# Kernel tuning notes

Measured on AMD Instinct MI355X. Metric: run time of the kernel, lower is better.

Reference implementation:

```python
import jax, jax.numpy as jnp
import numpy as np

# init kwargs baked as constants: crop_height -> depth dim, crop_length -> H, crop_width -> W
CROP_D, CROP_H, CROP_W = 16, 16, 16
EXTRAP = 0.0


def setup_inputs() -> dict:
    key = jax.random.key(0)
    k1, k2, k3 = jax.random.split(key, 3)
    N, C, D, H, W = 8, 32, 64, 64, 64
    NB = 256
    image = jax.random.normal(k1, (N, C, D, H, W), dtype=jnp.float32)
    # boxes: normalized (x1, y1, z1, x2, y2, z2) with lo <= hi per axis
    raw = jax.random.uniform(k2, (NB, 3, 2), dtype=jnp.float32)
    lo = jnp.min(raw, axis=2)
    hi = jnp.max(raw, axis=2)
    boxes = jnp.concatenate([lo, hi], axis=1)  # [NB, 6]
    box_ind = jax.random.randint(k3, (NB,), 0, N, dtype=jnp.int32)
    return {"image": image, "boxes": boxes, "box_ind": box_ind}


def _coords(lo, hi, L, c):
    # lo, hi: [nb] normalized box edges; returns [nb, c] continuous source coords
    if c > 1:
        i = jnp.arange(c, dtype=lo.dtype)
        step = (hi - lo) * (L - 1) / (c - 1)          # [nb]
        return lo[:, None] * (L - 1) + i[None, :] * step[:, None]
    return (0.5 * (lo + hi) * (L - 1))[:, None]


def _lerp_idx(coord, L):
    valid = (coord >= 0) & (coord <= L - 1)
    c = jnp.clip(coord, 0, L - 1)
    i0 = jnp.floor(c).astype(jnp.int32)
    i1 = jnp.minimum(i0 + 1, L - 1)
    frac = c - i0.astype(coord.dtype)
    return i0, i1, frac, valid


def reference(image, boxes, box_ind):
    N, C, D, H, W = image.shape
    x1, y1, z1, x2, y2, z2 = [boxes[:, k] for k in range(6)]
    zc = _coords(z1, z2, D, CROP_D)  # [nb, cd]
    yc = _coords(y1, y2, H, CROP_H)  # [nb, ch]
    xc = _coords(x1, x2, W, CROP_W)  # [nb, cw]
    z0, z1i, fz, vz = _lerp_idx(zc, D)
    y0, y1i, fy, vy = _lerp_idx(yc, H)
    x0, x1i, fx, vx = _lerp_idx(xc, W)

    img = jnp.moveaxis(image, 1, -1)  # [N, D, H, W, C] -> channels-last gather
    b = box_ind[:, None, None, None]

    def g(zi, yi, xi):
        # [nb, cd, ch, cw, C]
        return img[b, zi[:, :, None, None], yi[:, None, :, None], xi[:, None, None, :], :]

    fz_ = fz[:, :, None, None, None]
    fy_ = fy[:, None, :, None, None]
    fx_ = fx[:, None, None, :, None]

    c00 = g(z0, y0, x0) * (1 - fx_) + g(z0, y0, x1i) * fx_
    c01 = g(z0, y1i, x0) * (1 - fx_) + g(z0, y1i, x1i) * fx_
    c10 = g(z1i, y0, x0) * (1 - fx_) + g(z1i, y0, x1i) * fx_
    c11 = g(z1i, y1i, x0) * (1 - fx_) + g(z1i, y1i, x1i) * fx_
    c0 = c00 * (1 - fy_) + c01 * fy_
    c1 = c10 * (1 - fy_) + c11 * fy_
    out = c0 * (1 - fz_) + c1 * fz_  # [nb, cd, ch, cw, C]

    valid = (vz[:, :, None, None] & vy[:, None, :, None] & vx[:, None, None, :])[..., None]
    out = jnp.where(valid, out, jnp.asarray(EXTRAP, out.dtype))
    return jnp.moveaxis(out, -1, 1)  # [nb, C, cd, ch, cw]
```

## Files before the change

kernel.cpp:

```cpp
#include <hip/hip_runtime.h>

#define NBOX 256
#define NC   32
#define ND   64
#define NH   64
#define NW   64
#define CD   16
#define CH   16
#define CW   16
#define NXCD 8
#define HW_  (NH * NW)
#define DHW  (ND * NH * NW)
#define P    68

__global__ __launch_bounds__(256) void CropAndResize3D_89481348645400_kernel(
    const float* __restrict__ image,
    const float* __restrict__ boxes,
    const int*   __restrict__ box_ind,
    float*       __restrict__ out)
{
    __shared__ float sh[2][64 * P];

    const int nwg_per_xcd = (NBOX * CD) / NXCD;
    const int hw  = blockIdx.x;
    const int blk = (hw & (NXCD - 1)) * nwg_per_xcd + (hw >> 3);

    const int b = blk >> 4;
    const int z = blk & 15;
    const int t  = threadIdx.x;
    const int ty = t >> 4;
    const int tx = t & 15;

    const float bx1 = boxes[b*6+0], by1 = boxes[b*6+1], bz1 = boxes[b*6+2];
    const float bx2 = boxes[b*6+3], by2 = boxes[b*6+4], bz2 = boxes[b*6+5];
    const int   n   = box_ind[b];

    const float zstep = (bz2 - bz1) * 63.0f / 15.0f;
    const float ystep = (by2 - by1) * 63.0f / 15.0f;
    const float xstep = (bx2 - bx1) * 63.0f / 15.0f;

    const float zc = bz1 * 63.0f + (float)z * zstep;
    const bool  vz = (zc >= 0.0f) && (zc <= 63.0f);
    const float zq = fminf(fmaxf(zc, 0.0f), 63.0f);
    const int   z0 = (int)floorf(zq);
    const int   z1 = min(z0 + 1, ND - 1);
    const float fz = zq - (float)z0;

    const float yc = by1 * 63.0f + (float)ty * ystep;
    const bool  vy = (yc >= 0.0f) && (yc <= 63.0f);
    const float yq = fminf(fmaxf(yc, 0.0f), 63.0f);
    const float fy = yq - floorf(yq);

    const float xcf = bx1 * 63.0f + (float)tx * xstep;
    const bool  vx  = (xcf >= 0.0f) && (xcf <= 63.0f);
    const float xq  = fminf(fmaxf(xcf, 0.0f), 63.0f);
    const int   x0  = (int)floorf(xq);
    const int   x1  = min(x0 + 1, NW - 1);
    const float fx  = xq - (float)x0;

    const bool valid = vz && vy && vx;
    const float gz = 1.0f - fz, gy = 1.0f - fy, gx = 1.0f - fx;

    const float xcl = bx1 * 63.0f;
    const float xch = bx1 * 63.0f + 15.0f * xstep;
    const int x0min = (int)floorf(fminf(fmaxf(xcl, 0.0f), 63.0f));
    const int x1max = min((int)floorf(fminf(fmaxf(xch, 0.0f), 63.0f)) + 1, NW - 1);
    const int xlo4  = x0min & ~3;
    const int G     = ((x1max - xlo4) >> 2) + 1;
    const bool ld   = (tx < G);

    int soff[4], dst[4];
    #pragma unroll
    for (int k = 0; k < 4; ++k) {
        const int r   = k * 16 + ty;
        const int yo  = (r >> 1) & 15;
        const int yc_ = r & 1;
        const int zs  = (r >> 5) ? z1 : z0;
        const float yco = by1 * 63.0f + (float)yo * ystep;
        const float yqs = fminf(fmaxf(yco, 0.0f), 63.0f);
        const int   ys0 = (int)floorf(yqs);
        const int   ysel = yc_ ? min(ys0 + 1, NH - 1) : ys0;
        soff[k] = (zs * NH + ysel) * NW + xlo4 + tx * 4;
        dst[k]  = r * P + tx * 4;
    }

    const int dx0 = x0 - xlo4;
    const int dx1 = x1 - xlo4;
    const int a00 = (ty * 2 + 0) * P;
    const int a01 = (ty * 2 + 1) * P;
    const int a10 = (32 + ty * 2 + 0) * P;
    const int a11 = (32 + ty * 2 + 1) * P;

    const float* imgb = image + (size_t)n * (NC * DHW);
    float* op = out + (size_t)b * (NC * CD * CH * CW) + (z * CH + ty) * CW + tx;

    float4 A0, A1, A2, A3, B0, B1, B2, B3;

    #define ISSUE(Ra, Rb, Rc, Rd, c)  do { if (ld) {                         \
        const float* p_ = imgb + (size_t)(c) * DHW;                          \
        Ra = *(const float4*)(p_ + soff[0]);                                 \
        Rb = *(const float4*)(p_ + soff[1]);                                 \
        Rc = *(const float4*)(p_ + soff[2]);                                 \
        Rd = *(const float4*)(p_ + soff[3]); } } while (0)

    #define WRITE(Ra, Rb, Rc, Rd, buf)  do { if (ld) {                       \
        *(float4*)(sh[buf] + dst[0]) = Ra;                                   \
        *(float4*)(sh[buf] + dst[1]) = Rb;                                   \
        *(float4*)(sh[buf] + dst[2]) = Rc;                                   \
        *(float4*)(sh[buf] + dst[3]) = Rd; } } while (0)

    #define COMPUTE(buf, c)  do {                                            \
        const float* S_ = sh[buf];                                           \
        const float s000 = S_[a00 + dx0], s001 = S_[a00 + dx1];              \
        const float s010 = S_[a01 + dx0], s011 = S_[a01 + dx1];              \
        const float s100 = S_[a10 + dx0], s101 = S_[a10 + dx1];              \
        const float s110 = S_[a11 + dx0], s111 = S_[a11 + dx1];              \
        const float c00 = s000 * gx + s001 * fx;                             \
        const float c01 = s010 * gx + s011 * fx;                             \
        const float c10 = s100 * gx + s101 * fx;                             \
        const float c11 = s110 * gx + s111 * fx;                             \
        const float c0  = c00 * gy + c01 * fy;                               \
        const float c1  = c10 * gy + c11 * fy;                               \
        float v = c0 * gz + c1 * fz;                                         \
        v = valid ? v : 0.0f;                                                \
        __builtin_nontemporal_store(v, op + (c) * (CD * CH * CW));           \
    } while (0)

    ISSUE(A0, A1, A2, A3, 0);
    WRITE(A0, A1, A2, A3, 0);
    ISSUE(B0, B1, B2, B3, 1);
    __syncthreads();

    for (int c = 0; c < NC; c += 2) {
        if (c + 1 < NC) WRITE(B0, B1, B2, B3, 1);
        if (c + 2 < NC) ISSUE(A0, A1, A2, A3, c + 2);
        COMPUTE(0, c);
        __syncthreads();
        if (c + 1 < NC) {
            if (c + 2 < NC) WRITE(A0, A1, A2, A3, 0);
            if (c + 3 < NC) ISSUE(B0, B1, B2, B3, c + 3);
            COMPUTE(1, c + 1);
            __syncthreads();
        }
    }

    #undef ISSUE
    #undef WRITE
    #undef COMPUTE
}

extern "C" void kernel_launch(void* const* d_in, const int* in_sizes, int n_in,
                              void* d_out, int out_size, void* d_ws, size_t ws_size,
                              hipStream_t stream) {
    const float* image   = (const float*)d_in[0];
    const float* boxes   = (const float*)d_in[1];
    const int*   box_ind = (const int*)d_in[2];
    float*       out     = (float*)d_out;

    const int blocks = NBOX * CD;
    CropAndResize3D_89481348645400_kernel<<<blocks, 256, 0, stream>>>(
        image, boxes, box_ind, out);
}
```

Measured before the change: 124.4 us.

## Load image tiles directly into LDS with global_load_lds and XOR swizzle

Replaces the register-staged global-to-shared copy with direct global-to-LDS loads (global_load_lds, 16 bytes per lane). The padded LDS layout becomes an unpadded 64-wide layout with an XOR swizzle on the 4-float chunk index to avoid bank conflicts. Synchronisation is rewritten to use explicit vmcnt waits and two s_barriers per channel. The aim is to drop the VGPR round trip and the ds_write instructions. The cost is more barriers per iteration, and correctness depends on the wave-uniform LDS base matching the per-lane swizzle arithmetic.

```diff
diff --git a/kernel.cpp b/kernel.cpp
--- a/kernel.cpp
+++ b/kernel.cpp
@@ -1,4 +1,5 @@
 #include <hip/hip_runtime.h>
+#include <stdint.h>
 
 #define NBOX 256
 #define NC   32
@@ -9,9 +10,7 @@
 #define CH   16
 #define CW   16
 #define NXCD 8
-#define HW_  (NH * NW)
 #define DHW  (ND * NH * NW)
-#define P    68
 
 __global__ __launch_bounds__(256) void CropAndResize3D_89481348645400_kernel(
     const float* __restrict__ image,
@@ -19,7 +18,7 @@
     const int*   __restrict__ box_ind,
     float*       __restrict__ out)
 {
-    __shared__ float sh[2][64 * P];
+    __shared__ float sh[2 * 64 * 64];
 
     const int nwg_per_xcd = (NBOX * CD) / NXCD;
     const int hw  = blockIdx.x;
@@ -67,85 +66,106 @@
     const int x1max = min((int)floorf(fminf(fmaxf(xch, 0.0f), 63.0f)) + 1, NW - 1);
     const int xlo4  = x0min & ~3;
     const int G     = ((x1max - xlo4) >> 2) + 1;
-    const bool ld   = (tx < G);
 
-    int soff[4], dst[4];
-    #pragma unroll
-    for (int k = 0; k < 4; ++k) {
-        const int r   = k * 16 + ty;
-        const int yo  = (r >> 1) & 15;
-        const int yc_ = r & 1;
-        const int zs  = (r >> 5) ? z1 : z0;
-        const float yco = by1 * 63.0f + (float)yo * ystep;
-        const float yqs = fminf(fmaxf(yco, 0.0f), 63.0f);
-        const int   ys0 = (int)floorf(yqs);
-        const int   ysel = yc_ ? min(ys0 + 1, NH - 1) : ys0;
-        soff[k] = (zs * NH + ysel) * NW + xlo4 + tx * 4;
-        dst[k]  = r * P + tx * 4;
+    const int key = ty & 7;
+    const bool act = ((tx ^ key) < G);
+    const int sx  = xlo4 + ((tx ^ key) << 2);
+
+    int soff0, soff1, soff2, soff3;
+    {
+        int tmp[4];
+        #pragma unroll
+        for (int k = 0; k < 4; ++k) {
+            const int r   = k * 16 + ty;
+            const int yo  = (r >> 1) & 15;
+            const int yc_ = r & 1;
+            const int zs  = (r >> 5) ? z1 : z0;
+            const float yco = by1 * 63.0f + (float)yo * ystep;
+            const float yqs = fminf(fmaxf(yco, 0.0f), 63.0f);
+            const int   ys0 = (int)floorf(yqs);
+            const int   ysel = yc_ ? min(ys0 + 1, NH - 1) : ys0;
+            tmp[k] = (zs * NH + ysel) * NW + sx;
+        }
+        soff0 = tmp[0]; soff1 = tmp[1]; soff2 = tmp[2]; soff3 = tmp[3];
     }
+    const int wb    = (ty & ~3) * 64;
+    const int ldsb0 = wb;
+    const int ldsb1 = wb + 16 * 64;
+    const int ldsb2 = wb + 32 * 64;
+    const int ldsb3 = wb + 48 * 64;
 
     const int dx0 = x0 - xlo4;
     const int dx1 = x1 - xlo4;
-    const int a00 = (ty * 2 + 0) * P;
-    const int a01 = (ty * 2 + 1) * P;
-    const int a10 = (32 + ty * 2 + 0) * P;
-    const int a11 = (32 + ty * 2 + 1) * P;
+    #define IDX(r, dx) ((r) * 64 + (((((dx) >> 2) ^ ((r) & 7))) << 2) + ((dx) & 3))
+    const int a000 = IDX(2*ty    , dx0), a001 = IDX(2*ty    , dx1);
+    const int a010 = IDX(2*ty + 1, dx0), a011 = IDX(2*ty + 1, dx1);
+    const int a100 = IDX(32+2*ty , dx0), a101 = IDX(32+2*ty , dx1);
+    const int a110 = IDX(33+2*ty , dx0), a111 = IDX(33+2*ty , dx1);
+    #undef IDX
 
     const float* imgb = image + (size_t)n * (NC * DHW);
     float* op = out + (size_t)b * (NC * CD * CH * CW) + (z * CH + ty) * CW + tx;
 
-    float4 A0, A1, A2, A3, B0, B1, B2, B3;
+    #define ISSUE(c)  do { if (act) {                                          \
+        const float* p_ = imgb + (size_t)(c) * DHW;                            \
+        float* l_ = sh + (((c) & 1) << 12);                                    \
+        __builtin_amdgcn_global_load_lds(                                      \
+            (const __attribute__((address_space(1))) uint32_t*)(p_ + soff0),   \
+            (__attribute__((address_space(3))) uint32_t*)(l_ + ldsb0), 16, 0, 0); \
+        __builtin_amdgcn_global_load_lds(                                      \
+            (const __attribute__((address_space(1))) uint32_t*)(p_ + soff1),   \
+            (__attribute__((address_space(3))) uint32_t*)(l_ + ldsb1), 16, 0, 0); \
+        __builtin_amdgcn_global_load_lds(                                      \
+            (const __attribute__((address_space(1))) uint32_t*)(p_ + soff2),   \
+            (__attribute__((address_space(3))) uint32_t*)(l_ + ldsb2), 16, 0, 0); \
+        __builtin_amdgcn_global_load_lds(                                      \
+            (const __attribute__((address_space(1))) uint32_t*)(p_ + soff3),   \
+            (__attribute__((address_space(3))) uint32_t*)(l_ + ldsb3), 16, 0, 0); \
+    } } while (0)
 
-    #define ISSUE(Ra, Rb, Rc, Rd, c)  do { if (ld) {                         \
-        const float* p_ = imgb + (size_t)(c) * DHW;                          \
-        Ra = *(const float4*)(p_ + soff[0]);                                 \
-        Rb = *(const float4*)(p_ + soff[1]);                                 \
-        Rc = *(const float4*)(p_ + soff[2]);                                 \
-        Rd = *(const float4*)(p_ + soff[3]); } } while (0)
-
-    #define WRITE(Ra, Rb, Rc, Rd, buf)  do { if (ld) {                       \
-        *(float4*)(sh[buf] + dst[0]) = Ra;                                   \
-        *(float4*)(sh[buf] + dst[1]) = Rb;                                   \
-        *(float4*)(sh[buf] + dst[2]) = Rc;                                   \
-        *(float4*)(sh[buf] + dst[3]) = Rd; } } while (0)
-
-    #define COMPUTE(buf, c)  do {                                            \
-        const float* S_ = sh[buf];                                           \
-        const float s000 = S_[a00 + dx0], s001 = S_[a00 + dx1];              \
-        const float s010 = S_[a01 + dx0], s011 = S_[a01 + dx1];              \
-        const float s100 = S_[a10 + dx0], s101 = S_[a10 + dx1];              \
-        const float s110 = S_[a11 + dx0], s111 = S_[a11 + dx1];              \
-        const float c00 = s000 * gx + s001 * fx;                             \
-        const float c01 = s010 * gx + s011 * fx;                             \
-        const float c10 = s100 * gx + s101 * fx;                             \
-        const float c11 = s110 * gx + s111 * fx;                             \
-        const float c0  = c00 * gy + c01 * fy;                               \
-        const float c1  = c10 * gy + c11 * fy;                               \
-        float v = c0 * gz + c1 * fz;                                         \
-        v = valid ? v : 0.0f;                                                \
-        __builtin_nontemporal_store(v, op + (c) * (CD * CH * CW));           \
+    #define COMPUTE(c)  do {                                                   \
+        const float* S_ = sh + (((c) & 1) << 12);                              \
+        const float s000 = S_[a000], s001 = S_[a001];                          \
+        const float s010 = S_[a010], s011 = S_[a011];                          \
+        const float s100 = S_[a100], s101 = S_[a101];                          \
+        const float s110 = S_[a110], s111 = S_[a111];                          \
+        const float c00 = s000 * gx + s001 * fx;                               \
+        const float c01 = s010 * gx + s011 * fx;                               \
+        const float c10 = s100 * gx + s101 * fx;                               \
+        const float c11 = s110 * gx + s111 * fx;                               \
+        const float c0  = c00 * gy + c01 * fy;                                 \
+        const float c1  = c10 * gy + c11 * fy;                                 \
+        float v = c0 * gz + c1 * fz;                                           \
+        v = valid ? v : 0.0f;                                                  \
+        __builtin_nontemporal_store(v, op + (c) * (CD * CH * CW));             \
     } while (0)
 
-    ISSUE(A0, A1, A2, A3, 0);
-    WRITE(A0, A1, A2, A3, 0);
-    ISSUE(B0, B1, B2, B3, 1);
-    __syncthreads();
+    ISSUE(0);
+    ISSUE(1);
+    asm volatile("s_waitcnt vmcnt(4)" ::: "memory");
+    __builtin_amdgcn_s_barrier();
+    __builtin_amdgcn_sched_barrier(0);
 
-    for (int c = 0; c < NC; c += 2) {
-        if (c + 1 < NC) WRITE(B0, B1, B2, B3, 1);
-        if (c + 2 < NC) ISSUE(A0, A1, A2, A3, c + 2);
-        COMPUTE(0, c);
-        __syncthreads();
+    #pragma unroll 2
+    for (int c = 0; c < NC; ++c) {
+        COMPUTE(c);
         if (c + 1 < NC) {
-            if (c + 2 < NC) WRITE(A0, A1, A2, A3, 0);
-            if (c + 3 < NC) ISSUE(B0, B1, B2, B3, c + 3);
-            COMPUTE(1, c + 1);
-            __syncthreads();
+            __builtin_amdgcn_sched_barrier(0);
+            __builtin_amdgcn_s_barrier();
+            __builtin_amdgcn_sched_barrier(0);
+            if (c + 2 < NC) {
+                ISSUE(c + 2);
+                asm volatile("s_waitcnt vmcnt(4)" ::: "memory");
+            } else {
+                asm volatile("s_waitcnt vmcnt(0)" ::: "memory");
+            }
+            __builtin_amdgcn_sched_barrier(0);
+            __builtin_amdgcn_s_barrier();
+            __builtin_amdgcn_sched_barrier(0);
         }
     }
 
     #undef ISSUE
-    #undef WRITE
     #undef COMPUTE
 }
 
```

Result: no change. 124.2 us (-0.2%).
